# Performance work log

Measured on AMD Instinct MI355X. Metric: run time of the kernel, lower is better.

Reference implementation:

```python
import jax, jax.numpy as jnp
import numpy as np

B, D, UD = 32, 1024, 256          # batch, chunks_dim, units_dim
ENT, NENT = 32, 64                # entity_size, n_entities
S, C = NENT * ENT, NENT + 1       # src_len (units), n_chunks
NEG_INF = float('-inf')


def setup_inputs() -> dict:
    key = jax.random.key(0)
    ks = jax.random.split(key, 9)
    source = jax.random.normal(ks[0], (B, D), jnp.float32)
    high_level_repr = jax.random.normal(ks[1], (C, B, D), jnp.float32)
    pos_embs = jax.random.normal(ks[2], (S, B, UD), jnp.float32)
    low_level_repr = jax.random.normal(ks[3], (S, B, D), jnp.float32)
    low_level_mask = jax.random.randint(ks[4], (NENT, B, ENT), 0, 2).astype(bool)
    high_level_mask = jax.random.randint(ks[5], (1, B, C), 0, 2).astype(bool)
    high_level_mask = high_level_mask.at[..., 0].set(False)  # avoid all-masked chunk softmax
    W_unit = jax.random.normal(ks[6], (UD, D), jnp.float32) / np.sqrt(D)
    W_chunk = jax.random.normal(ks[7], (D, D), jnp.float32) / np.sqrt(D)
    W_out = jax.random.normal(ks[8], (D, 2 * D), jnp.float32) / np.sqrt(2 * D)
    return {"source": source, "high_level_repr": high_level_repr, "pos_embs": pos_embs,
            "low_level_repr": low_level_repr, "low_level_mask": low_level_mask,
            "high_level_mask": high_level_mask, "W_unit": W_unit, "W_chunk": W_chunk,
            "W_out": W_out}


def reference(source, high_level_repr, pos_embs, low_level_repr,
              low_level_mask, high_level_mask, W_unit, W_chunk, W_out):
    # batch-first views (torch transposes(0,1))
    hl = jnp.swapaxes(high_level_repr, 0, 1)    # (B, C, D)
    ll = jnp.swapaxes(low_level_repr, 0, 1)     # (B, S, D)
    pe = jnp.swapaxes(pos_embs, 0, 1)           # (B, S, UD)
    ll_mask = jnp.swapaxes(low_level_mask, 0, 1)   # (B, NENT, ENT)
    hl_mask = jnp.swapaxes(high_level_mask, 0, 1)  # (B, 1, C)

    # 'general' attention scorers, tgt_len == 1
    q_u = source @ W_unit.T                      # (B, UD)
    align_units = jnp.einsum('bd,bsd->bs', q_u, pe)        # (B, S)
    q_c = source @ W_chunk.T                     # (B, D)
    align_chunks = jnp.einsum('bd,bcd->bc', q_c, hl)[:, None, :]  # (B, 1, C)

    # low-level masked softmax per entity, NaN rows -> 0
    au = align_units.reshape(B, NENT, ENT)
    au = jnp.where(ll_mask, NEG_INF, au)
    au = jax.nn.softmax(au, axis=-1)
    all_masked = jnp.all(ll_mask, axis=-1)       # (B, NENT) rows that were NaN
    au = jnp.where(all_masked[..., None], 0.0, au)
    au = au.reshape(B, 1, S)

    # high-level masked softmax, drop chunk 0, inflate to unit granularity
    ac = jnp.where(hl_mask, NEG_INF, align_chunks)
    ac = jax.nn.softmax(ac, axis=-1)[:, :, 1:]   # (B, 1, C-1)
    ac_inflated = jnp.repeat(ac, ENT, axis=-1)   # (B, 1, S)

    align_vectors = ac_inflated * au             # (B, 1, S)
    c = jnp.einsum('bts,bsd->btd', align_vectors, ll)  # (B, 1, D)
    concat = jnp.concatenate([c, source[:, None, :]], axis=-1).reshape(B, 2 * D)
    attn_h = jnp.tanh(concat @ W_out.T)          # (B, D); tanh since attn_type='general'

    return (attn_h,
            align_vectors[:, 0, :],              # (B, S)
            ac[:, 0, :],                         # (B, C-1)
            au.reshape(B, S))                    # (B, S)
```

## Files before the change

### kernel.cpp

```cpp
#include <hip/hip_runtime.h>

#define B 32
#define D 1024
#define UD 256
#define ENT 32
#define NENT 64
#define S 2048
#define C 65
#define NSLAB 8

__device__ __forceinline__ float dot4(float4 w, const float* q) {
    return w.x * q[0] + w.y * q[1] + w.z * q[2] + w.w * q[3];
}

__global__ __launch_bounds__(256) void k_proj(const float* __restrict__ src,
                                              const float* __restrict__ Wu,
                                              const float* __restrict__ Wc,
                                              float* __restrict__ qu,
                                              float* __restrict__ qc) {
    __shared__ alignas(16) float s_src[4][D];
    __shared__ float red[4][64][4];
    int t = threadIdx.x, rg = blockIdx.x, bg = blockIdx.y;
    for (int f = t; f < 4 * (D / 4); f += 256) {
        int bb = f >> 8, i4 = f & 255;
        float4 v = *(const float4*)(src + (size_t)(bg * 4 + bb) * D + i4 * 4);
        *(float4*)(&s_src[bb][i4 * 4]) = v;
    }
    __syncthreads();
    int jl = t & 63, kq = t >> 6;
    int gj = rg * 64 + jl;
    const float* wrow = (gj < UD) ? (Wu + (size_t)gj * D) : (Wc + (size_t)(gj - UD) * D);
    const float4* wp = (const float4*)wrow + kq * 64;
    float acc[4] = {0.f, 0.f, 0.f, 0.f};
#pragma unroll 4
    for (int i = 0; i < 64; ++i) {
        float4 w = wp[i];
        int k = kq * 256 + i * 4;
#pragma unroll
        for (int bb = 0; bb < 4; ++bb) acc[bb] += dot4(w, &s_src[bb][k]);
    }
#pragma unroll
    for (int bb = 0; bb < 4; ++bb) red[kq][jl][bb] = acc[bb];
    __syncthreads();
    {
        int jl2 = t & 63, bb = t >> 6;
        float s = red[0][jl2][bb] + red[1][jl2][bb] + red[2][jl2][bb] + red[3][jl2][bb];
        int gj2 = rg * 64 + jl2, b = bg * 4 + bb;
        if (gj2 < UD) qu[b * UD + gj2] = s;
        else qc[b * D + (gj2 - UD)] = s;
    }
}

__global__ __launch_bounds__(256) void k_score(const float* __restrict__ hl,
                                               const float* __restrict__ qc,
                                               float* __restrict__ sc) {
    __shared__ float red[4];
    int c = blockIdx.x, b = blockIdx.y, t = threadIdx.x;
    const float4* hp = (const float4*)(hl + ((size_t)c * B + b) * D);
    const float4* qp = (const float4*)(qc + (size_t)b * D);
    float4 h = hp[t];
    float4 q = qp[t];
    float acc = h.x * q.x + h.y * q.y + h.z * q.z + h.w * q.w;
    for (int o = 32; o >= 1; o >>= 1) acc += __shfl_xor(acc, o);
    if ((t & 63) == 0) red[t >> 6] = acc;
    __syncthreads();
    if (t == 0) sc[b * C + c] = red[0] + red[1] + red[2] + red[3];
}

__global__ __launch_bounds__(512) void k_fused(const float* __restrict__ pe,
                                               const float* __restrict__ ll,
                                               const int* __restrict__ lmask,
                                               const int* __restrict__ hmask,
                                               const float* __restrict__ qu,
                                               const float* __restrict__ sc,
                                               float* __restrict__ pf,
                                               float* __restrict__ out_au,
                                               float* __restrict__ out_ac,
                                               float* __restrict__ out_av) {
    __shared__ alignas(16) float4 s_part[NSLAB][256];
    int ss = blockIdx.x, b = blockIdx.y, t = threadIdx.x;
    int w = t >> 6, l = t & 63;
    int n = ss * NSLAB + w;

    bool m1 = hmask[b * C + l] != 0;
    float x1 = m1 ? -1e30f : sc[b * C + l];
    bool m2 = hmask[b * C + 64] != 0;
    float x2 = m2 ? -1e30f : sc[b * C + 64];
    float mx = x1;
    for (int o = 32; o >= 1; o >>= 1) mx = fmaxf(mx, __shfl_xor(mx, o));
    mx = fmaxf(mx, x2);
    float e1 = m1 ? 0.f : __expf(x1 - mx);
    float sm = e1;
    for (int o = 32; o >= 1; o >>= 1) sm += __shfl_xor(sm, o);
    float e2 = m2 ? 0.f : __expf(x2 - mx);
    sm += e2;
    int c = n + 1;
    float en = (c < 64) ? __shfl(e1, c) : e2;
    float ac = en / sm;
    if (l == 0) out_ac[b * NENT + n] = ac;

    float4 qf = ((const float4*)(qu + (size_t)b * UD))[l];
    int s0 = n * ENT;
    const float4* pe4 = (const float4*)pe;
    float score = 0.f;
#pragma unroll 4
    for (int j = 0; j < ENT; ++j) {
        float4 v = pe4[((size_t)(s0 + j) * B + b) * (UD / 4) + l];
        float p = v.x * qf.x + v.y * qf.y + v.z * qf.z + v.w * qf.w;
        for (int o = 32; o >= 1; o >>= 1) p += __shfl_xor(p, o);
        score = (l == j) ? p : score;
    }

    int e = l & 31;
    bool m = lmask[((size_t)n * B + b) * ENT + e] != 0;
    float v = m ? -1e30f : score;
    float emx = v;
    for (int o = 16; o >= 1; o >>= 1) emx = fmaxf(emx, __shfl_xor(emx, o));
    float p = m ? 0.f : __expf(v - emx);
    float esm = p;
    for (int o = 16; o >= 1; o >>= 1) esm += __shfl_xor(esm, o);
    float au = (esm > 0.f) ? p / esm : 0.f;
    float av = ac * au;
    if (l < ENT) {
        out_au[b * S + s0 + l] = au;
        out_av[b * S + s0 + l] = av;
    }

    float4 a0 = {0.f, 0.f, 0.f, 0.f}, a1 = a0, a2 = a0, a3 = a0;
    const float4* ll4 = (const float4*)ll;
#pragma unroll 4
    for (int j = 0; j < ENT; ++j) {
        float wv = __shfl(av, j);
        const float4* rp = ll4 + ((size_t)(s0 + j) * B + b) * (D / 4) + l;
        float4 x0 = rp[0], x1v = rp[64], x2v = rp[128], x3v = rp[192];
        a0.x += wv * x0.x;  a0.y += wv * x0.y;  a0.z += wv * x0.z;  a0.w += wv * x0.w;
        a1.x += wv * x1v.x; a1.y += wv * x1v.y; a1.z += wv * x1v.z; a1.w += wv * x1v.w;
        a2.x += wv * x2v.x; a2.y += wv * x2v.y; a2.z += wv * x2v.z; a2.w += wv * x2v.w;
        a3.x += wv * x3v.x; a3.y += wv * x3v.y; a3.z += wv * x3v.z; a3.w += wv * x3v.w;
    }
    s_part[w][l] = a0;
    s_part[w][64 + l] = a1;
    s_part[w][128 + l] = a2;
    s_part[w][192 + l] = a3;
    __syncthreads();

    if (t < 256) {
        float4 r = {0.f, 0.f, 0.f, 0.f};
#pragma unroll
        for (int ww = 0; ww < NSLAB; ++ww) {
            float4 x = s_part[ww][t];
            r.x += x.x; r.y += x.y; r.z += x.z; r.w += x.w;
        }
        *(float4*)(pf + ((size_t)ss * B + b) * D + t * 4) = r;
    }
}

__global__ __launch_bounds__(256) void k_out(const float* __restrict__ Wo,
                                             const float* __restrict__ src,
                                             const float* __restrict__ pf,
                                             float* __restrict__ out_h) {
    __shared__ alignas(16) float cc[4][2 * D];
    __shared__ float red[4][64][4];
    int t = threadIdx.x, jg = blockIdx.x, bg = blockIdx.y;
    for (int f = t; f < 4 * (2 * D / 4); f += 256) {
        int bb = f >> 9, part = f & 511;
        int b = bg * 4 + bb;
        float4 v;
        if (part < 256) {
            float4 a = {0.f, 0.f, 0.f, 0.f};
            const float4* pp = (const float4*)(pf + (size_t)b * D) + part;
#pragma unroll
            for (int ssi = 0; ssi < NSLAB; ++ssi) {
                float4 x = pp[(size_t)ssi * (B * D / 4)];
                a.x += x.x; a.y += x.y; a.z += x.z; a.w += x.w;
            }
            v = a;
        } else {
            v = *(const float4*)(src + (size_t)b * D + (part - 256) * 4);
        }
        *(float4*)(&cc[bb][part * 4]) = v;
    }
    __syncthreads();
    int jl = t & 63, kq = t >> 6;
    int j = jg * 64 + jl;
    const float4* wp = (const float4*)(Wo + (size_t)j * 2 * D) + kq * 128;
    float acc[4] = {0.f, 0.f, 0.f, 0.f};
#pragma unroll 4
    for (int i = 0; i < 128; ++i) {
        float4 w = wp[i];
        int k = kq * 512 + i * 4;
#pragma unroll
        for (int bb = 0; bb < 4; ++bb) acc[bb] += dot4(w, &cc[bb][k]);
    }
#pragma unroll
    for (int bb = 0; bb < 4; ++bb) red[kq][jl][bb] = acc[bb];
    __syncthreads();
    {
        int jl2 = t & 63, bb = t >> 6;
        float s = red[0][jl2][bb] + red[1][jl2][bb] + red[2][jl2][bb] + red[3][jl2][bb];
        out_h[(size_t)(bg * 4 + bb) * D + jg * 64 + jl2] = tanhf(s);
    }
}

extern "C" void kernel_launch(void* const* d_in, const int* in_sizes, int n_in,
                              void* d_out, int out_size, void* d_ws, size_t ws_size,
                              hipStream_t stream) {
    const float* src = (const float*)d_in[0];
    const float* hl = (const float*)d_in[1];
    const float* pe = (const float*)d_in[2];
    const float* ll = (const float*)d_in[3];
    const int* lmask = (const int*)d_in[4];
    const int* hmask = (const int*)d_in[5];
    const float* Wu = (const float*)d_in[6];
    const float* Wc = (const float*)d_in[7];
    const float* Wo = (const float*)d_in[8];

    float* out = (float*)d_out;
    float* out_h = out;
    float* out_av = out + B * D;
    float* out_ac = out_av + B * S;
    float* out_au = out_ac + B * NENT;

    float* ws = (float*)d_ws;
    float* qu = ws;
    float* qc = qu + B * UD;
    float* scb = qc + B * D;
    float* pf = scb + B * C;

    k_proj<<<dim3(20, 8), 256, 0, stream>>>(src, Wu, Wc, qu, qc);
    k_score<<<dim3(C, B), 256, 0, stream>>>(hl, qc, scb);
    k_fused<<<dim3(NSLAB, B), 512, 0, stream>>>(pe, ll, lmask, hmask, qu, scb,
                                                pf, out_au, out_ac, out_av);
    k_out<<<dim3(16, 8), 256, 0, stream>>>(Wo, src, pf, out_h);
}
```

Before: 459.1 us.

## Fuse chunk scoring into main kernel and double grid slabs

Removes the separate chunk-score kernel. Each block of the fused kernel now computes all 65 chunk scores for its batch row into shared memory before running the chunk softmax. Blocks shrink from 512 to 256 threads (4 entities each), and the slab count doubles to 16, giving twice as many blocks to spread the large low-level and positional-embedding streams across more CUs. The trade-off is that every one of the 16 blocks per batch row re-reads that row's high-level representation, about 16x redundant traffic that mostly has to be served from cache. The output kernel must also reduce over twice as many partial slabs.

```diff
diff --git a/kernel.cpp b/kernel.cpp
--- a/kernel.cpp
+++ b/kernel.cpp
@@ -7,7 +7,7 @@
 #define NENT 64
 #define S 2048
 #define C 65
-#define NSLAB 8
+#define NSLAB 16
 
 __device__ __forceinline__ float dot4(float4 w, const float* q) {
     return w.x * q[0] + w.y * q[1] + w.z * q[2] + w.w * q[3];
@@ -51,41 +51,44 @@
     }
 }
 
-__global__ __launch_bounds__(256) void k_score(const float* __restrict__ hl,
-                                               const float* __restrict__ qc,
-                                               float* __restrict__ sc) {
-    __shared__ float red[4];
-    int c = blockIdx.x, b = blockIdx.y, t = threadIdx.x;
-    const float4* hp = (const float4*)(hl + ((size_t)c * B + b) * D);
-    const float4* qp = (const float4*)(qc + (size_t)b * D);
-    float4 h = hp[t];
-    float4 q = qp[t];
-    float acc = h.x * q.x + h.y * q.y + h.z * q.z + h.w * q.w;
-    for (int o = 32; o >= 1; o >>= 1) acc += __shfl_xor(acc, o);
-    if ((t & 63) == 0) red[t >> 6] = acc;
-    __syncthreads();
-    if (t == 0) sc[b * C + c] = red[0] + red[1] + red[2] + red[3];
-}
-
-__global__ __launch_bounds__(512) void k_fused(const float* __restrict__ pe,
+__global__ __launch_bounds__(256) void k_fused(const float* __restrict__ pe,
                                                const float* __restrict__ ll,
+                                               const float* __restrict__ hl,
                                                const int* __restrict__ lmask,
                                                const int* __restrict__ hmask,
                                                const float* __restrict__ qu,
-                                               const float* __restrict__ sc,
+                                               const float* __restrict__ qc,
                                                float* __restrict__ pf,
                                                float* __restrict__ out_au,
                                                float* __restrict__ out_ac,
                                                float* __restrict__ out_av) {
-    __shared__ alignas(16) float4 s_part[NSLAB][256];
+    __shared__ float s_sc[C];
+    __shared__ alignas(16) float4 s_part[4][256];
     int ss = blockIdx.x, b = blockIdx.y, t = threadIdx.x;
     int w = t >> 6, l = t & 63;
-    int n = ss * NSLAB + w;
+    int n = ss * 4 + w;
+    int s0 = n * ENT;
+
+    {
+        const float4* qc4 = (const float4*)(qc + (size_t)b * D);
+        float4 q0 = qc4[l], q1 = qc4[l + 64], q2 = qc4[l + 128], q3 = qc4[l + 192];
+        for (int c = w; c < C; c += 4) {
+            const float4* hp = (const float4*)(hl + ((size_t)c * B + b) * D);
+            float4 h0 = hp[l], h1 = hp[l + 64], h2 = hp[l + 128], h3 = hp[l + 192];
+            float acc = h0.x * q0.x + h0.y * q0.y + h0.z * q0.z + h0.w * q0.w
+                      + h1.x * q1.x + h1.y * q1.y + h1.z * q1.z + h1.w * q1.w
+                      + h2.x * q2.x + h2.y * q2.y + h2.z * q2.z + h2.w * q2.w
+                      + h3.x * q3.x + h3.y * q3.y + h3.z * q3.z + h3.w * q3.w;
+            for (int o = 32; o >= 1; o >>= 1) acc += __shfl_xor(acc, o);
+            if (l == 0) s_sc[c] = acc;
+        }
+    }
+    __syncthreads();
 
     bool m1 = hmask[b * C + l] != 0;
-    float x1 = m1 ? -1e30f : sc[b * C + l];
+    float x1 = m1 ? -1e30f : s_sc[l];
     bool m2 = hmask[b * C + 64] != 0;
-    float x2 = m2 ? -1e30f : sc[b * C + 64];
+    float x2 = m2 ? -1e30f : s_sc[64];
     float mx = x1;
     for (int o = 32; o >= 1; o >>= 1) mx = fmaxf(mx, __shfl_xor(mx, o));
     mx = fmaxf(mx, x2);
@@ -100,7 +103,6 @@
     if (l == 0) out_ac[b * NENT + n] = ac;
 
     float4 qf = ((const float4*)(qu + (size_t)b * UD))[l];
-    int s0 = n * ENT;
     const float4* pe4 = (const float4*)pe;
     float score = 0.f;
 #pragma unroll 4
@@ -144,10 +146,10 @@
     s_part[w][192 + l] = a3;
     __syncthreads();
 
-    if (t < 256) {
+    {
         float4 r = {0.f, 0.f, 0.f, 0.f};
 #pragma unroll
-        for (int ww = 0; ww < NSLAB; ++ww) {
+        for (int ww = 0; ww < 4; ++ww) {
             float4 x = s_part[ww][t];
             r.x += x.x; r.y += x.y; r.z += x.z; r.w += x.w;
         }
@@ -224,12 +226,10 @@
     float* ws = (float*)d_ws;
     float* qu = ws;
     float* qc = qu + B * UD;
-    float* scb = qc + B * D;
-    float* pf = scb + B * C;
+    float* pf = qc + B * D;
 
     k_proj<<<dim3(20, 8), 256, 0, stream>>>(src, Wu, Wc, qu, qc);
-    k_score<<<dim3(C, B), 256, 0, stream>>>(hl, qc, scb);
-    k_fused<<<dim3(NSLAB, B), 512, 0, stream>>>(pe, ll, lmask, hmask, qu, scb,
+    k_fused<<<dim3(NSLAB, B), 256, 0, stream>>>(pe, ll, hl, lmask, hmask, qu, qc,
                                                 pf, out_au, out_ac, out_av);
     k_out<<<dim3(16, 8), 256, 0, stream>>>(Wo, src, pf, out_h);
 }
```

Result: slower. 471.7 us (+2.8%).
